# Performance work log

Measured on AMD Instinct MI355X. Metric: run time of the kernel, lower is better.

The kernel has to match this reference:

```python
import jax, jax.numpy as jnp
import numpy as np

N, D = 262144, 256
MARGIN = 0.75


def setup_inputs() -> dict:
    key = jax.random.key(0)
    k1, k2 = jax.random.split(key)
    feature_results = jax.random.normal(k1, (N, D), dtype=jnp.float32)
    target_var = jax.random.uniform(k2, (N,), dtype=jnp.float32)
    return {"feature_results": feature_results, "target_var": target_var}


def reference(feature_results, target_var):
    t = target_var
    # 4 engagement-level masks, [4, N]
    masks = jnp.stack([
        t <= 0.1,
        (t > 0.3) & (t <= 0.4),
        (t > 0.6) & (t <= 0.7),
        (t > 0.8) & (t <= 1.1),
    ]).astype(feature_results.dtype)
    counts = masks.sum(axis=1)                      # [4]
    sums = masks @ feature_results                  # [4, D] masked group sums
    # mean if the group is non-empty, else keep zeros (matches the torch code)
    means = jnp.where(counts[:, None] > 0, sums / jnp.maximum(counts, 1.0)[:, None], 0.0)

    def dist(i, j):
        return jnp.linalg.norm(means[i] - means[j])

    d12, d13, d14 = dist(0, 1), dist(0, 2), dist(0, 3)
    d23, d24, d34 = dist(1, 2), dist(1, 3), dist(2, 3)
    m = MARGIN
    loss = (jax.nn.relu(d12 - d13 + m) + jax.nn.relu(d12 - d14 + 2 * m)
            + jax.nn.relu(d23 - d24 + m) + jax.nn.relu(d23 - d14 + 2 * m)
            + jax.nn.relu(d34 - d24 + m) + jax.nn.relu(d34 - d14 + 2 * m))
    return loss
```

## Files before the change

### kernel.cpp

```cpp
#include <hip/hip_runtime.h>
#include <math.h>

#define D 256
#define COPY_FLOATS 1028
#define NCOPIES_MAX 32

__device__ __forceinline__ int classify(float t) {
    if (t <= 0.1f) return 0;
    if (t > 0.3f && t <= 0.4f) return 1;
    if (t > 0.6f && t <= 0.7f) return 2;
    if (t > 0.8f && t <= 1.1f) return 3;
    return -1;
}

__global__ __launch_bounds__(256) void group_partial(
    const float* __restrict__ F, const float* __restrict__ T,
    float* __restrict__ ws, int nRows, int ncopies)
{
    __shared__ float lsum[4][4][D];
    __shared__ float lcnt[4][4];

    const int tid  = threadIdx.x;
    const int lane = tid & 63;
    const int wav  = tid >> 6;
    const int waveId = blockIdx.x * 4 + wav;
    const int nWaves = gridDim.x * 4;

    float4 a0 = {0.f,0.f,0.f,0.f}, a1 = a0, a2 = a0, a3 = a0;
    float c0 = 0.f, c1 = 0.f, c2 = 0.f, c3 = 0.f;

    for (long long base = (long long)waveId * 32; base < (long long)nRows;
         base += (long long)nWaves * 32) {
        const long long r = base + (lane & 31);
        const float t = (r < (long long)nRows) ? T[r] : 2.0f;
        const int g = classify(t);

        unsigned m0 = (unsigned)__ballot(g == 0);
        unsigned m1 = (unsigned)__ballot(g == 1);
        unsigned m2 = (unsigned)__ballot(g == 2);
        unsigned m3 = (unsigned)__ballot(g == 3);
        m0 = __builtin_amdgcn_readfirstlane(m0);
        m1 = __builtin_amdgcn_readfirstlane(m1);
        m2 = __builtin_amdgcn_readfirstlane(m2);
        m3 = __builtin_amdgcn_readfirstlane(m3);

        c0 += (float)__popc(m0);
        c1 += (float)__popc(m1);
        c2 += (float)__popc(m2);
        c3 += (float)__popc(m3);

        const float* Fb = F + (size_t)base * D + (size_t)lane * 4;
        while (m0) {
            const int j = __ffs(m0) - 1; m0 &= m0 - 1;
            const float4 v = *reinterpret_cast<const float4*>(Fb + (size_t)j * D);
            a0.x += v.x; a0.y += v.y; a0.z += v.z; a0.w += v.w;
        }
        while (m1) {
            const int j = __ffs(m1) - 1; m1 &= m1 - 1;
            const float4 v = *reinterpret_cast<const float4*>(Fb + (size_t)j * D);
            a1.x += v.x; a1.y += v.y; a1.z += v.z; a1.w += v.w;
        }
        while (m2) {
            const int j = __ffs(m2) - 1; m2 &= m2 - 1;
            const float4 v = *reinterpret_cast<const float4*>(Fb + (size_t)j * D);
            a2.x += v.x; a2.y += v.y; a2.z += v.z; a2.w += v.w;
        }
        while (m3) {
            const int j = __ffs(m3) - 1; m3 &= m3 - 1;
            const float4 v = *reinterpret_cast<const float4*>(Fb + (size_t)j * D);
            a3.x += v.x; a3.y += v.y; a3.z += v.z; a3.w += v.w;
        }
    }

    *reinterpret_cast<float4*>(&lsum[wav][0][lane * 4]) = a0;
    *reinterpret_cast<float4*>(&lsum[wav][1][lane * 4]) = a1;
    *reinterpret_cast<float4*>(&lsum[wav][2][lane * 4]) = a2;
    *reinterpret_cast<float4*>(&lsum[wav][3][lane * 4]) = a3;
    if (lane == 0) {
        lcnt[wav][0] = c0; lcnt[wav][1] = c1; lcnt[wav][2] = c2; lcnt[wav][3] = c3;
    }
    __syncthreads();

    float* dst = ws + (size_t)(blockIdx.x % ncopies) * COPY_FLOATS;
#pragma unroll
    for (int g = 0; g < 4; ++g) {
        const float s = lsum[0][g][tid] + lsum[1][g][tid]
                      + lsum[2][g][tid] + lsum[3][g][tid];
        atomicAdd(dst + g * D + tid, s);
    }
    if (tid < 4) {
        const float c = lcnt[0][tid] + lcnt[1][tid] + lcnt[2][tid] + lcnt[3][tid];
        atomicAdd(dst + 4 * D + tid, c);
    }
}

__global__ __launch_bounds__(256) void finalize(
    const float* __restrict__ ws, int ncopies, float* __restrict__ out)
{
    const int tid  = threadIdx.x;
    const int lane = tid & 63;
    const int wav  = tid >> 6;

    float s[4] = {0.f,0.f,0.f,0.f};
    float c[4] = {0.f,0.f,0.f,0.f};
    for (int cp = 0; cp < ncopies; ++cp) {
        const float* w = ws + (size_t)cp * COPY_FLOATS;
#pragma unroll
        for (int g = 0; g < 4; ++g) {
            s[g] += w[g * D + tid];
            c[g] += w[4 * D + g];
        }
    }

    float m[4];
#pragma unroll
    for (int g = 0; g < 4; ++g)
        m[g] = (c[g] > 0.f) ? s[g] / fmaxf(c[g], 1.f) : 0.f;

    float p[6];
    p[0] = (m[0]-m[1]) * (m[0]-m[1]);
    p[1] = (m[0]-m[2]) * (m[0]-m[2]);
    p[2] = (m[0]-m[3]) * (m[0]-m[3]);
    p[3] = (m[1]-m[2]) * (m[1]-m[2]);
    p[4] = (m[1]-m[3]) * (m[1]-m[3]);
    p[5] = (m[2]-m[3]) * (m[2]-m[3]);

    __shared__ float red[6][4];
#pragma unroll
    for (int k = 0; k < 6; ++k) {
        float v = p[k];
#pragma unroll
        for (int off = 32; off >= 1; off >>= 1)
            v += __shfl_down(v, off, 64);
        if (lane == 0) red[k][wav] = v;
    }
    __syncthreads();

    if (tid == 0) {
        float d[6];
#pragma unroll
        for (int k = 0; k < 6; ++k)
            d[k] = sqrtf(red[k][0] + red[k][1] + red[k][2] + red[k][3]);
        const float d12 = d[0], d13 = d[1], d14 = d[2];
        const float d23 = d[3], d24 = d[4], d34 = d[5];
        const float M = 0.75f;
        auto relu = [](float x) { return x > 0.f ? x : 0.f; };
        const float loss = relu(d12 - d13 + M)        + relu(d12 - d14 + 2.f * M)
                         + relu(d23 - d24 + M)        + relu(d23 - d14 + 2.f * M)
                         + relu(d34 - d24 + M)        + relu(d34 - d14 + 2.f * M);
        out[0] = loss;
    }
}

extern "C" void kernel_launch(void* const* d_in, const int* in_sizes, int n_in,
                              void* d_out, int out_size, void* d_ws, size_t ws_size,
                              hipStream_t stream) {
    const float* F = (const float*)d_in[0];
    const float* T = (const float*)d_in[1];
    float* out = (float*)d_out;
    const int nRows = in_sizes[1];

    int ncopies = (int)(ws_size / (COPY_FLOATS * sizeof(float)));
    if (ncopies > NCOPIES_MAX) ncopies = NCOPIES_MAX;
    if (ncopies < 1) ncopies = 1;

    hipMemsetAsync(d_ws, 0, (size_t)ncopies * COPY_FLOATS * sizeof(float), stream);

    const int blocks = 2048;
    group_partial<<<blocks, 256, 0, stream>>>(F, T, (float*)d_ws, nRows, ncopies);
    finalize<<<1, 256, 0, stream>>>((const float*)d_ws, ncopies, out);
}
```

Baseline: 51.83 us.

## Process 64 rows per wave and batch four row loads across merged group masks

```diff
diff --git a/kernel.cpp b/kernel.cpp
--- a/kernel.cpp
+++ b/kernel.cpp
@@ -4,14 +4,7 @@
 #define D 256
 #define COPY_FLOATS 1028
 #define NCOPIES_MAX 32
-
-__device__ __forceinline__ int classify(float t) {
-    if (t <= 0.1f) return 0;
-    if (t > 0.3f && t <= 0.4f) return 1;
-    if (t > 0.6f && t <= 0.7f) return 2;
-    if (t > 0.8f && t <= 1.1f) return 3;
-    return -1;
-}
+#define GRID_BLOCKS 1024
 
 __global__ __launch_bounds__(256) void group_partial(
     const float* __restrict__ F, const float* __restrict__ T,
@@ -23,52 +16,57 @@
     const int tid  = threadIdx.x;
     const int lane = tid & 63;
     const int wav  = tid >> 6;
-    const int waveId = blockIdx.x * 4 + wav;
-    const int nWaves = gridDim.x * 4;
+    const long long waveId = (long long)blockIdx.x * 4 + wav;
+    const long long nWaves = (long long)gridDim.x * 4;
 
     float4 a0 = {0.f,0.f,0.f,0.f}, a1 = a0, a2 = a0, a3 = a0;
     float c0 = 0.f, c1 = 0.f, c2 = 0.f, c3 = 0.f;
 
-    for (long long base = (long long)waveId * 32; base < (long long)nRows;
-         base += (long long)nWaves * 32) {
-        const long long r = base + (lane & 31);
+    for (long long base = waveId * 64; base < (long long)nRows;
+         base += nWaves * 64) {
+        const long long r = base + lane;
         const float t = (r < (long long)nRows) ? T[r] : 2.0f;
-        const int g = classify(t);
 
-        unsigned m0 = (unsigned)__ballot(g == 0);
-        unsigned m1 = (unsigned)__ballot(g == 1);
-        unsigned m2 = (unsigned)__ballot(g == 2);
-        unsigned m3 = (unsigned)__ballot(g == 3);
-        m0 = __builtin_amdgcn_readfirstlane(m0);
-        m1 = __builtin_amdgcn_readfirstlane(m1);
-        m2 = __builtin_amdgcn_readfirstlane(m2);
-        m3 = __builtin_amdgcn_readfirstlane(m3);
+        const unsigned long long m0 = __ballot(t <= 0.1f);
+        const unsigned long long m1 = __ballot(t > 0.3f && t <= 0.4f);
+        const unsigned long long m2 = __ballot(t > 0.6f && t <= 0.7f);
+        const unsigned long long m3 = __ballot(t > 0.8f && t <= 1.1f);
 
-        c0 += (float)__popc(m0);
-        c1 += (float)__popc(m1);
-        c2 += (float)__popc(m2);
-        c3 += (float)__popc(m3);
+        c0 += (float)__popcll(m0);
+        c1 += (float)__popcll(m1);
+        c2 += (float)__popcll(m2);
+        c3 += (float)__popcll(m3);
 
         const float* Fb = F + (size_t)base * D + (size_t)lane * 4;
-        while (m0) {
-            const int j = __ffs(m0) - 1; m0 &= m0 - 1;
-            const float4 v = *reinterpret_cast<const float4*>(Fb + (size_t)j * D);
-            a0.x += v.x; a0.y += v.y; a0.z += v.z; a0.w += v.w;
+        unsigned long long mAll = m0 | m1 | m2 | m3;
+
+        auto addRow = [&](int jj, const float4& v) {
+            if ((m0 >> jj) & 1ull) {
+                a0.x += v.x; a0.y += v.y; a0.z += v.z; a0.w += v.w;
+            } else if ((m1 >> jj) & 1ull) {
+                a1.x += v.x; a1.y += v.y; a1.z += v.z; a1.w += v.w;
+            } else if ((m2 >> jj) & 1ull) {
+                a2.x += v.x; a2.y += v.y; a2.z += v.z; a2.w += v.w;
+            } else {
+                a3.x += v.x; a3.y += v.y; a3.z += v.z; a3.w += v.w;
+            }
+        };
+
+        while (__popcll(mAll) >= 4) {
+            const int j0 = __ffsll(mAll) - 1; mAll &= mAll - 1;
+            const int j1 = __ffsll(mAll) - 1; mAll &= mAll - 1;
+            const int j2 = __ffsll(mAll) - 1; mAll &= mAll - 1;
+            const int j3 = __ffsll(mAll) - 1; mAll &= mAll - 1;
+            const float4 v0 = *reinterpret_cast<const float4*>(Fb + (size_t)j0 * D);
+            const float4 v1 = *reinterpret_cast<const float4*>(Fb + (size_t)j1 * D);
+            const float4 v2 = *reinterpret_cast<const float4*>(Fb + (size_t)j2 * D);
+            const float4 v3 = *reinterpret_cast<const float4*>(Fb + (size_t)j3 * D);
+            addRow(j0, v0); addRow(j1, v1); addRow(j2, v2); addRow(j3, v3);
         }
-        while (m1) {
-            const int j = __ffs(m1) - 1; m1 &= m1 - 1;
-            const float4 v = *reinterpret_cast<const float4*>(Fb + (size_t)j * D);
-            a1.x += v.x; a1.y += v.y; a1.z += v.z; a1.w += v.w;
-        }
-        while (m2) {
-            const int j = __ffs(m2) - 1; m2 &= m2 - 1;
-            const float4 v = *reinterpret_cast<const float4*>(Fb + (size_t)j * D);
-            a2.x += v.x; a2.y += v.y; a2.z += v.z; a2.w += v.w;
-        }
-        while (m3) {
-            const int j = __ffs(m3) - 1; m3 &= m3 - 1;
-            const float4 v = *reinterpret_cast<const float4*>(Fb + (size_t)j * D);
-            a3.x += v.x; a3.y += v.y; a3.z += v.z; a3.w += v.w;
+        while (mAll) {
+            const int j0 = __ffsll(mAll) - 1; mAll &= mAll - 1;
+            const float4 v0 = *reinterpret_cast<const float4*>(Fb + (size_t)j0 * D);
+            addRow(j0, v0);
         }
     }
 
@@ -103,6 +101,7 @@
 
     float s[4] = {0.f,0.f,0.f,0.f};
     float c[4] = {0.f,0.f,0.f,0.f};
+#pragma unroll 4
     for (int cp = 0; cp < ncopies; ++cp) {
         const float* w = ws + (size_t)cp * COPY_FLOATS;
 #pragma unroll
@@ -144,10 +143,10 @@
         const float d12 = d[0], d13 = d[1], d14 = d[2];
         const float d23 = d[3], d24 = d[4], d34 = d[5];
         const float M = 0.75f;
-        auto relu = [](float x) { return x > 0.f ? x : 0.f; };
-        const float loss = relu(d12 - d13 + M)        + relu(d12 - d14 + 2.f * M)
-                         + relu(d23 - d24 + M)        + relu(d23 - d14 + 2.f * M)
-                         + relu(d34 - d24 + M)        + relu(d34 - d14 + 2.f * M);
+        const float loss =
+              fmaxf(d12 - d13 + M, 0.f)       + fmaxf(d12 - d14 + 2.f * M, 0.f)
+            + fmaxf(d23 - d24 + M, 0.f)       + fmaxf(d23 - d14 + 2.f * M, 0.f)
+            + fmaxf(d34 - d24 + M, 0.f)       + fmaxf(d34 - d14 + 2.f * M, 0.f);
         out[0] = loss;
     }
 }
@@ -166,7 +165,6 @@
 
     hipMemsetAsync(d_ws, 0, (size_t)ncopies * COPY_FLOATS * sizeof(float), stream);
 
-    const int blocks = 2048;
-    group_partial<<<blocks, 256, 0, stream>>>(F, T, (float*)d_ws, nRows, ncopies);
+    group_partial<<<GRID_BLOCKS, 256, 0, stream>>>(F, T, (float*)d_ws, nRows, ncopies);
     finalize<<<1, 256, 0, stream>>>((const float*)d_ws, ncopies, out);
 }
```

Result: faster. 45.34 us (-12.5%).
